# Kernel tuning notes

Hardware: AMD Instinct MI355X
Metric: run time of the kernel (lower is better)

## Reference

```python
import jax, jax.numpy as jnp
import numpy as np


def _lstm(x, Wx, Wh, b):
    """Fused-gate LSTM over time axis 1. x: [B,T,I]; Wx: [I,4H]; Wh: [H,4H]; b: [4H].
    Gate order (i, f, g, o) as in flax.linen.LSTMCell. Zero initial carry."""
    B, T, _ = x.shape
    H = Wh.shape[0]
    # Precompute all input-to-gate contributions in one big GEMM.
    xg = jnp.einsum('bti,ih->bth', x, Wx) + b  # [B,T,4H]

    def step(carry, xt):
        c, h = carry
        z = xt + h @ Wh  # [B,4H]
        i, f, g, o = jnp.split(z, 4, axis=-1)
        c = jax.nn.sigmoid(f) * c + jax.nn.sigmoid(i) * jnp.tanh(g)
        h = jax.nn.sigmoid(o) * jnp.tanh(c)
        return (c, h), h

    init = (jnp.zeros((B, H), x.dtype), jnp.zeros((B, H), x.dtype))
    _, hs = jax.lax.scan(step, init, jnp.swapaxes(xg, 0, 1))  # hs: [T,B,H]
    return jnp.swapaxes(hs, 0, 1)  # [B,T,H]


def _forward(X, conv_w, conv_b,
             Wx1, Wh1, b1, Wx2, Wh2, b2, Wx3, Wh3, b3, Wx4, Wh4, b4,
             Wa, ba, Va, bva, Wd1, bd1, Wd2, bd2):
    # 1-D conv, SAME padding (flax default), NWC layout.
    x = jax.lax.conv_general_dilated(X, conv_w, (1,), 'SAME',
                                     dimension_numbers=('NWC', 'WIO', 'NWC')) + conv_b
    # NOTE: source uses jnp.flip(..., axis=-1) -> flips FEATURE axis (faithful to source).
    x1 = _lstm(x, Wx1, Wh1, b1)
    x2 = _lstm(jnp.flip(x, axis=-1), Wx2, Wh2, b2)
    x = jnp.concatenate([x1, x2], axis=-1)  # [B,T,2F]
    x1 = _lstm(x, Wx3, Wh3, b3)
    x2 = _lstm(jnp.flip(x, axis=-1), Wx4, Wh4, b4)
    enc = jnp.concatenate([x1, x2], axis=-1)  # [B,T,4F]
    # Additive attention: softmax over time axis.
    score = jnp.tanh(enc @ Wa + ba) @ Va + bva  # [B,T,1]
    w = jax.nn.softmax(score, axis=1)
    ctx = jnp.sum(w * enc, axis=1)  # [B,4F]
    # MLP head (dropout deterministic -> identity).
    h = jnp.tanh(ctx @ Wd1 + bd1)
    return h @ Wd2 + bd2  # [B,1]


def setup_inputs() -> dict:
    key = jax.random.key(0)
    B, T, Cin, F = 32, 4096, 8, 64
    ks = iter(jax.random.split(key, 32))

    def w(shape):
        fan_in = shape[0] if len(shape) <= 2 else shape[0] * shape[1]
        return jax.random.normal(next(ks), shape, jnp.float32) / np.sqrt(fan_in)

    d = {}
    d['X'] = jax.random.normal(next(ks), (B, T, Cin), jnp.float32)
    d['conv_w'] = w((4, Cin, 16))
    d['conv_b'] = jnp.zeros((16,), jnp.float32)
    lstm_dims = {'1': (16, F), '2': (16, F), '3': (2 * F, 2 * F), '4': (2 * F, 2 * F)}
    for n, (i_dim, h_dim) in lstm_dims.items():
        d['Wx' + n] = w((i_dim, 4 * h_dim))
        d['Wh' + n] = w((h_dim, 4 * h_dim))
        d['b' + n] = jnp.zeros((4 * h_dim,), jnp.float32)
    d['Wa'] = w((4 * F, F)); d['ba'] = jnp.zeros((F,), jnp.float32)
    d['Va'] = w((F, 1));     d['bva'] = jnp.zeros((1,), jnp.float32)
    d['Wd1'] = w((4 * F, F)); d['bd1'] = jnp.zeros((F,), jnp.float32)
    d['Wd2'] = w((F, 1));     d['bd2'] = jnp.zeros((1,), jnp.float32)
    d['deterministic'] = 1
    return d


def reference(X, conv_w, conv_b,
              Wx1, Wh1, b1, Wx2, Wh2, b2, Wx3, Wh3, b3, Wx4, Wh4, b4,
              Wa, ba, Va, bva, Wd1, bd1, Wd2, bd2, deterministic):
    # deterministic=1 -> dropout is the identity; already reflected in _forward.
    return _forward(X, conv_w, conv_b,
                    Wx1, Wh1, b1, Wx2, Wh2, b2, Wx3, Wh3, b3, Wx4, Wh4, b4,
                    Wa, ba, Va, bva, Wd1, bd1, Wd2, bd2)
```

## Files before the change

kernel.cpp:

```cpp
#include <hip/hip_runtime.h>


#define TFULL 4096
#define NB 32

__device__ __forceinline__ float fexp2(float x){ return __builtin_amdgcn_exp2f(x); }
__device__ __forceinline__ float frcp(float x){ return __builtin_amdgcn_rcpf(x); }
__device__ __forceinline__ float sigf(float x){ return frcp(1.f + fexp2(-1.44269504f*x)); }
__device__ __forceinline__ float tanh_(float x){
    float e = fexp2(fminf(2.88539008f*x, 126.f));
    return (e - 1.f) * frcp(e + 1.f);
}
#define PIN4(v) asm volatile("" : "+v"(v.x), "+v"(v.y), "+v"(v.z), "+v"(v.w))

__global__ __launch_bounds__(256) void k_init(float* __restrict__ st1,
        float* __restrict__ st2, float* __restrict__ am, float* __restrict__ al,
        float* __restrict__ acc){
    int i = blockIdx.x * 256 + threadIdx.x;
    if (i < 8192)  st1[i] = 0.f;
    if (i < 16384) st2[i] = 0.f;
    if (i < 8192)  acc[i] = 0.f;
    if (i < 32){ am[i] = -3.4e38f; al[i] = 0.f; }
}

__global__ __launch_bounds__(256) void k_pack(
        const float* __restrict__ Wx1, const float* __restrict__ Wh1, const float* __restrict__ b1,
        const float* __restrict__ Wx2, const float* __restrict__ Wh2, const float* __restrict__ b2,
        const float* __restrict__ Wx3, const float* __restrict__ Wh3, const float* __restrict__ b3,
        const float* __restrict__ Wx4, const float* __restrict__ Wh4, const float* __restrict__ b4,
        float* __restrict__ W34, float* __restrict__ b34, float* __restrict__ W2p,
        float* __restrict__ W1p, float* __restrict__ b12i){
    int i0 = blockIdx.x * 256 + threadIdx.x;
    int stride = gridDim.x * 256;
    for (int e = i0; e < 131072; e += stride){
        int k = e >> 10, n = e & 1023;
        int l = n >> 9, nn = n & 511, j = nn >> 2, g = nn & 3;
        W34[e] = l ? Wx4[(127 - k)*512 + g*128 + j] : Wx3[k*512 + g*128 + j];
    }
    for (int e = i0; e < 1024; e += stride){
        int l = e >> 9, nn = e & 511, j = nn >> 2, g = nn & 3;
        b34[e] = (l ? b4 : b3)[g*128 + j];
    }
    for (int e = i0; e < 131072; e += stride){
        int l = e >> 16, r = e & 65535, tid = r >> 6, widx = r & 63;
        int q = tid & 127, s = tid >> 7;
        int m = widx >> 4, kk = widx & 15;
        W2p[e] = (l ? Wh4 : Wh3)[(16*s + kk)*512 + m*128 + q];
    }
    for (int e = i0; e < 49152; e += stride){
        int l = e / 24576, r = e % 24576, tid = r / 48, widx = r % 48;
        int q = tid & 63, s = tid >> 6;
        int m = widx / 12, rem = widx % 12, k4 = rem >> 2, cmp = rem & 3;
        float v = 0.f;
        if (k4 < 2){
            v = (l ? Wh2 : Wh1)[(8*s + k4*4 + cmp)*256 + m*64 + q];
        } else if (s < 4){
            int rr = 4*s + cmp;
            v = l ? Wx2[(15 - rr)*256 + m*64 + q] : Wx1[rr*256 + m*64 + q];
        }
        W1p[e] = v;
    }
    for (int e = i0; e < 512; e += stride){
        int l = e >> 8, nn = e & 255, j = nn >> 2, g = nn & 3;
        b12i[e] = (l ? b2 : b1)[g*64 + j];
    }
}

__global__ __launch_bounds__(256) void k_conv(const float* __restrict__ X,
        const float* __restrict__ W, const float* __restrict__ Bv,
        float* __restrict__ out, int t0, int lc){
    __shared__ float Ws[512];
    __shared__ float bs[16];
    int tid = threadIdx.x;
    Ws[tid] = W[tid]; Ws[tid + 256] = W[tid + 256];
    if (tid < 16) bs[tid] = Bv[tid];
    __syncthreads();
    int m = blockIdx.x * 256 + tid;
    int b = m >> lc, trel = m & ((1 << lc) - 1);
    int t = t0 + trel;
    float o[16];
    #pragma unroll
    for (int co = 0; co < 16; ++co) o[co] = bs[co];
    #pragma unroll
    for (int w = 0; w < 4; ++w){
        int tt = t + w - 1;
        if (tt >= 0 && tt < TFULL){
            const float* xr = X + ((size_t)(b << 12) + tt) * 8;
            #pragma unroll
            for (int ci = 0; ci < 8; ++ci){
                float v = xr[ci];
                #pragma unroll
                for (int co = 0; co < 16; ++co) o[co] += v * Ws[(w*8 + ci)*16 + co];
            }
        }
    }
    float* op = out + (size_t)m * 16;
    #pragma unroll
    for (int q = 0; q < 4; ++q)
        *(float4*)(op + q*4) = make_float4(o[q*4], o[q*4+1], o[q*4+2], o[q*4+3]);
}

__global__ void __launch_bounds__(512)
k_scan1(const float* __restrict__ x, const float* __restrict__ W1p,
        const float* __restrict__ b12i,
        float* __restrict__ cc, float* __restrict__ st1, int C){
    int l = blockIdx.x >> 5;
    int b = blockIdx.x & 31;
    int tid = threadIdx.x;
    int q = tid & 63;
    int s = tid >> 6;
    float4 w[12];
    {
        const float4* wp = (const float4*)(W1p + ((size_t)l*512 + tid)*48);
        #pragma unroll
        for (int i = 0; i < 12; ++i) w[i] = wp[i];
        #pragma unroll
        for (int i = 0; i < 12; ++i) PIN4(w[i]);
    }
    float4 bi4 = make_float4(0.f, 0.f, 0.f, 0.f);
    if (tid < 64) bi4 = *(const float4*)(b12i + l*256 + tid*4);

    __shared__ float xs[128 * 16];
    __shared__ float zp1[8 * 256];
    __shared__ float ccbuf[128 * 64];
    __shared__ float hbufs[64];
    float c = 0.f;
    int sidx = (l*32 + b)*64 + q;
    if (tid < 64){ c = st1[sidx]; hbufs[tid] = st1[4096 + sidx]; }
    __syncthreads();

    const float* xb = x + ((size_t)b * C) * 16;
    float* ccb = cc + ((size_t)b * C) * 128 + (l << 6);
    int BS = C < 128 ? C : 128;
    int bsm = BS - 1;
    int fr = tid >> 2, fi = tid & 3;

    #pragma clang loop unroll(disable)
    for (int t = 0; t < C; ++t){
        int st = t & bsm;
        if (st == 0){
            __syncthreads();
            if (t && fr < BS){
                const float4* cb4 = (const float4*)ccbuf + fr*16 + fi*4;
                float4* cgp = (float4*)(ccb + (size_t)(t - BS + fr)*128) + fi*4;
                #pragma unroll
                for (int i = 0; i < 4; ++i) cgp[i] = cb4[i];
            }
            if (tid < BS*4)
                ((float4*)xs)[tid] = ((const float4*)(xb + (size_t)t*16))[tid];
            __syncthreads();
        }
        float a0 = 0.f, a1 = 0.f, a2 = 0.f, a3 = 0.f;
        const float4* hb4 = (const float4*)hbufs + (s << 1);
        #pragma unroll
        for (int k4 = 0; k4 < 2; ++k4){
            float4 hv = hb4[k4];
            a0 = fmaf(hv.x, w[k4].x, a0);     a0 = fmaf(hv.y, w[k4].y, a0);
            a0 = fmaf(hv.z, w[k4].z, a0);     a0 = fmaf(hv.w, w[k4].w, a0);
            a1 = fmaf(hv.x, w[3+k4].x, a1);   a1 = fmaf(hv.y, w[3+k4].y, a1);
            a1 = fmaf(hv.z, w[3+k4].z, a1);   a1 = fmaf(hv.w, w[3+k4].w, a1);
            a2 = fmaf(hv.x, w[6+k4].x, a2);   a2 = fmaf(hv.y, w[6+k4].y, a2);
            a2 = fmaf(hv.z, w[6+k4].z, a2);   a2 = fmaf(hv.w, w[6+k4].w, a2);
            a3 = fmaf(hv.x, w[9+k4].x, a3);   a3 = fmaf(hv.y, w[9+k4].y, a3);
            a3 = fmaf(hv.z, w[9+k4].z, a3);   a3 = fmaf(hv.w, w[9+k4].w, a3);
        }
        if (s < 4){
            float4 xv = ((const float4*)(xs + st * 16))[s];
            a0 = fmaf(xv.x, w[2].x, a0);    a0 = fmaf(xv.y, w[2].y, a0);
            a0 = fmaf(xv.z, w[2].z, a0);    a0 = fmaf(xv.w, w[2].w, a0);
            a1 = fmaf(xv.x, w[5].x, a1);    a1 = fmaf(xv.y, w[5].y, a1);
            a1 = fmaf(xv.z, w[5].z, a1);    a1 = fmaf(xv.w, w[5].w, a1);
            a2 = fmaf(xv.x, w[8].x, a2);    a2 = fmaf(xv.y, w[8].y, a2);
            a2 = fmaf(xv.z, w[8].z, a2);    a2 = fmaf(xv.w, w[8].w, a2);
            a3 = fmaf(xv.x, w[11].x, a3);   a3 = fmaf(xv.y, w[11].y, a3);
            a3 = fmaf(xv.z, w[11].z, a3);   a3 = fmaf(xv.w, w[11].w, a3);
        }
        *(float4*)(zp1 + (s << 8) + (q << 2)) = make_float4(a0, a1, a2, a3);
        __syncthreads();
        if (tid < 64){
            float4 z = bi4;
            #pragma unroll
            for (int ss = 0; ss < 8; ++ss){
                float4 p = *(const float4*)(zp1 + (ss << 8) + (q << 2));
                z.x += p.x; z.y += p.y; z.z += p.z; z.w += p.w;
            }
            float gi = sigf(z.x), gf = sigf(z.y), gg = tanh_(z.z), go = sigf(z.w);
            c = gf * c + gi * gg;
            float h = go * tanh_(c);
            hbufs[tid] = h;
            ccbuf[st*64 + tid] = h;
        }
        __syncthreads();
    }
    if (fr < BS){
        const float4* cb4 = (const float4*)ccbuf + fr*16 + fi*4;
        float4* cgp = (float4*)(ccb + (size_t)(C - BS + fr)*128) + fi*4;
        #pragma unroll
        for (int i = 0; i < 4; ++i) cgp[i] = cb4[i];
    }
    if (tid < 64){ st1[sidx] = c; st1[4096 + sidx] = hbufs[tid]; }
}

template<bool TANH>
__global__ __launch_bounds__(128) void k_gemm(
        const float* __restrict__ A, int lda,
        const float* __restrict__ B, int ldb,
        const float* __restrict__ bias,
        float* __restrict__ Cm, int ldc, int K){
    __shared__ float As[64 * 129];
    __shared__ float Bs[64 * 68];
    int tid = threadIdx.x;
    int tx = tid & 7;
    int ty = tid >> 3;
    int r0 = blockIdx.x * 128;
    int n0 = blockIdx.y * 64;
    float acc[8][8];
    #pragma unroll
    for (int i = 0; i < 8; ++i)
        #pragma unroll
        for (int n = 0; n < 8; ++n) acc[i][n] = 0.f;

    for (int kb = 0; kb < K; kb += 64){
        __syncthreads();
        for (int idx = tid; idx < 2048; idx += 128){
            int r = idx >> 4, k4 = idx & 15;
            float4 v = *(const float4*)(A + (size_t)(r0 + r) * lda + kb + k4*4);
            As[(k4*4 + 0)*129 + r] = v.x;
            As[(k4*4 + 1)*129 + r] = v.y;
            As[(k4*4 + 2)*129 + r] = v.z;
            As[(k4*4 + 3)*129 + r] = v.w;
        }
        for (int idx = tid; idx < 1024; idx += 128){
            int n4 = idx & 15, k = idx >> 4;
            float4 v = *(const float4*)(B + (size_t)(kb + k) * ldb + n0 + n4*4);
            *(float4*)(Bs + k*68 + n4*4) = v;
        }
        __syncthreads();
        #pragma unroll 4
        for (int k = 0; k < 64; ++k){
            float a[8];
            #pragma unroll
            for (int i = 0; i < 8; ++i) a[i] = As[k*129 + ty*8 + i];
            float4 b0 = *(const float4*)(Bs + k*68 + tx*8);
            float4 b1 = *(const float4*)(Bs + k*68 + tx*8 + 4);
            float bq[8] = {b0.x, b0.y, b0.z, b0.w, b1.x, b1.y, b1.z, b1.w};
            #pragma unroll
            for (int i = 0; i < 8; ++i)
                #pragma unroll
                for (int n = 0; n < 8; ++n) acc[i][n] += a[i] * bq[n];
        }
    }
    #pragma unroll
    for (int i = 0; i < 8; ++i){
        size_t rr = (size_t)r0 + ty*8 + i;
        float* cp = Cm + rr * ldc + n0 + tx*8;
        float ov[8];
        #pragma unroll
        for (int n = 0; n < 8; ++n){
            float v = acc[i][n] + bias[n0 + tx*8 + n];
            ov[n] = TANH ? tanh_(v) : v;
        }
        *(float4*)cp       = make_float4(ov[0], ov[1], ov[2], ov[3]);
        *(float4*)(cp + 4) = make_float4(ov[4], ov[5], ov[6], ov[7]);
    }
}

__global__ void __launch_bounds__(1024)
k_scan2(const float* __restrict__ xg, const float* __restrict__ W2p,
        float* __restrict__ enc, float* __restrict__ st2, int C){
    int l = blockIdx.x >> 5;
    int b = blockIdx.x & 31;
    int tid = threadIdx.x;
    int q = tid & 127;
    int s = tid >> 7;
    float4 w[16];
    {
        const float4* wp = (const float4*)(W2p + ((size_t)l*1024 + tid)*64);
        #pragma unroll
        for (int i = 0; i < 16; ++i) w[i] = wp[i];
        #pragma unroll
        for (int i = 0; i < 16; ++i) PIN4(w[i]);
    }

    __shared__ float xgbuf[32 * 512];
    __shared__ float zp[8 * 512];
    __shared__ float encbuf[32 * 128];
    __shared__ float hbufs[128];

    float c = 0.f;
    int sidx = (l*32 + b)*128 + q;
    if (tid < 128){ c = st2[sidx]; hbufs[tid] = st2[8192 + sidx]; }
    __syncthreads();

    const float* xgg = xg + ((size_t)b * C) * 1024 + (l << 9);
    float* encb = enc + ((size_t)b * C) * 256 + (l << 7);
    int tq = tid & 31, tr = tid >> 5;

    #pragma clang loop unroll(disable)
    for (int t = 0; t < C; ++t){
        int st = t & 31;
        if (st == 0){
            __syncthreads();
            if (t){
                float4 ev = *(const float4*)(encbuf + tr*128 + tq*4);
                *(float4*)(encb + (size_t)(t - 32 + tr) * 256 + tq*4) = ev;
            }
            {
                const float4* src = (const float4*)(xgg + (size_t)(t + tr) * 1024);
                float4* xb4 = (float4*)(xgbuf + tr*512);
                #pragma unroll
                for (int i = 0; i < 4; ++i) xb4[tq + 32*i] = src[tq + 32*i];
            }
            __syncthreads();
        }
        float a0 = 0.f, a1 = 0.f, a2 = 0.f, a3 = 0.f;
        const float4* hb4 = (const float4*)hbufs + (s << 2);
        #pragma unroll
        for (int k4 = 0; k4 < 4; ++k4){
            float4 hv = hb4[k4];
            a0 = fmaf(hv.x, w[k4].x, a0);      a0 = fmaf(hv.y, w[k4].y, a0);
            a0 = fmaf(hv.z, w[k4].z, a0);      a0 = fmaf(hv.w, w[k4].w, a0);
            a1 = fmaf(hv.x, w[4+k4].x, a1);    a1 = fmaf(hv.y, w[4+k4].y, a1);
            a1 = fmaf(hv.z, w[4+k4].z, a1);    a1 = fmaf(hv.w, w[4+k4].w, a1);
            a2 = fmaf(hv.x, w[8+k4].x, a2);    a2 = fmaf(hv.y, w[8+k4].y, a2);
            a2 = fmaf(hv.z, w[8+k4].z, a2);    a2 = fmaf(hv.w, w[8+k4].w, a2);
            a3 = fmaf(hv.x, w[12+k4].x, a3);   a3 = fmaf(hv.y, w[12+k4].y, a3);
            a3 = fmaf(hv.z, w[12+k4].z, a3);   a3 = fmaf(hv.w, w[12+k4].w, a3);
        }
        *(float4*)(zp + (s << 9) + (q << 2)) = make_float4(a0, a1, a2, a3);
        __syncthreads();
        if (tid < 128){
            float4 z = *(const float4*)(xgbuf + (st << 9) + (q << 2));
            #pragma unroll
            for (int ss = 0; ss < 8; ++ss){
                float4 p = *(const float4*)(zp + (ss << 9) + (q << 2));
                z.x += p.x; z.y += p.y; z.z += p.z; z.w += p.w;
            }
            float gi = sigf(z.x), gf = sigf(z.y), gg = tanh_(z.z), go = sigf(z.w);
            c = gf * c + gi * gg;
            float h = go * tanh_(c);
            hbufs[tid] = h;
            encbuf[st*128 + tid] = h;
        }
        __syncthreads();
    }
    {
        float4 ev = *(const float4*)(encbuf + tr*128 + tq*4);
        *(float4*)(encb + (size_t)(C - 32 + tr) * 256 + tq*4) = ev;
    }
    if (tid < 128){ st2[sidx] = c; st2[8192 + sidx] = hbufs[tid]; }
}

__global__ __launch_bounds__(256) void k_scorev(const float* __restrict__ u,
        const float* __restrict__ Va, const float* __restrict__ bva,
        float* __restrict__ sc){
    int m = blockIdx.x * 256 + threadIdx.x;
    const float4* up = (const float4*)(u + (size_t)m * 64);
    const float4* vp = (const float4*)Va;
    float acc = 0.f;
    #pragma unroll
    for (int i = 0; i < 16; ++i){
        float4 v = up[i], w = vp[i];
        acc += v.x*w.x + v.y*w.y + v.z*w.z + v.w*w.w;
    }
    sc[m] = acc + bva[0];
}

__global__ __launch_bounds__(1024) void k_attn(const float* __restrict__ sc,
        const float* __restrict__ enc, float* __restrict__ am,
        float* __restrict__ al, float* __restrict__ acc, int C){
    int b = blockIdx.x, tid = threadIdx.x;
    __shared__ float es[1024];
    __shared__ float red[16];
    __shared__ float sh[2];
    const float* sp = sc + (size_t)b * C;
    float mloc = -3.4e38f;
    for (int t = tid; t < C; t += 1024) mloc = fmaxf(mloc, sp[t]);
    #pragma unroll
    for (int off = 32; off; off >>= 1) mloc = fmaxf(mloc, __shfl_down(mloc, off));
    if ((tid & 63) == 0) red[tid >> 6] = mloc;
    __syncthreads();
    if (tid == 0){
        float mc = -3.4e38f;
        #pragma unroll
        for (int i = 0; i < 16; ++i) mc = fmaxf(mc, red[i]);
        float mo = am[b];
        float mn = fmaxf(mo, mc);
        sh[0] = mn;
        sh[1] = fexp2(1.44269504f * (mo - mn));
        am[b] = mn;
    }
    __syncthreads();
    float mn = sh[0], alpha = sh[1];
    float eloc = 0.f;
    for (int t = tid; t < C; t += 1024){
        float e = fexp2(1.44269504f * (sp[t] - mn));
        es[t] = e; eloc += e;
    }
    #pragma unroll
    for (int off = 32; off; off >>= 1) eloc += __shfl_down(eloc, off);
    if ((tid & 63) == 0) red[tid >> 6] = eloc;
    __syncthreads();
    if (tid == 0){
        float sm = 0.f;
        #pragma unroll
        for (int i = 0; i < 16; ++i) sm += red[i];
        al[b] = al[b] * alpha + sm;
    }
    int jf = tid & 255, sl = tid >> 8;
    int tlen = C >> 2;
    const float* ep = enc + ((size_t)b * C + (size_t)sl * tlen) * 256 + jf;
    const float* eb = es + sl * tlen;
    float a = 0.f;
    for (int t = 0; t < tlen; ++t) a = fmaf(eb[t], ep[(size_t)t * 256], a);
    __syncthreads();
    es[tid] = a;
    __syncthreads();
    if (tid < 256)
        acc[b*256 + tid] = acc[b*256 + tid] * alpha
                         + ((es[tid] + es[256 + tid]) + (es[512 + tid] + es[768 + tid]));
}

__global__ __launch_bounds__(256) void k_head(const float* __restrict__ acc,
        const float* __restrict__ al,
        const float* __restrict__ Wd1, const float* __restrict__ bd1,
        const float* __restrict__ Wd2, const float* __restrict__ bd2,
        float* __restrict__ out){
    __shared__ float ctxs[32 * 256];
    __shared__ float h1s[32 * 64];
    int tid = threadIdx.x;
    for (int idx = tid; idx < 8192; idx += 256){
        int b = idx >> 8;
        ctxs[idx] = acc[idx] / al[b];
    }
    __syncthreads();
    for (int idx = tid; idx < 2048; idx += 256){
        int b = idx >> 6, n = idx & 63;
        float a = bd1[n];
        for (int i = 0; i < 256; ++i) a += ctxs[b*256 + i] * Wd1[i*64 + n];
        h1s[idx] = tanh_(a);
    }
    __syncthreads();
    if (tid < 32){
        float a = bd2[0];
        #pragma unroll
        for (int n = 0; n < 64; ++n) a += h1s[tid*64 + n] * Wd2[n];
        out[tid] = a;
    }
}

extern "C" void kernel_launch(void* const* d_in, const int* in_sizes, int n_in,
                              void* d_out, int out_size, void* d_ws, size_t ws_size,
                              hipStream_t stream){
    const float* X     = (const float*)d_in[0];
    const float* convw = (const float*)d_in[1];
    const float* convb = (const float*)d_in[2];
    const float* Wx1 = (const float*)d_in[3];
    const float* Wh1 = (const float*)d_in[4];
    const float* b1  = (const float*)d_in[5];
    const float* Wx2 = (const float*)d_in[6];
    const float* Wh2 = (const float*)d_in[7];
    const float* b2  = (const float*)d_in[8];
    const float* Wx3 = (const float*)d_in[9];
    const float* Wh3 = (const float*)d_in[10];
    const float* b3  = (const float*)d_in[11];
    const float* Wx4 = (const float*)d_in[12];
    const float* Wh4 = (const float*)d_in[13];
    const float* b4  = (const float*)d_in[14];
    const float* Wa  = (const float*)d_in[15];
    const float* ba  = (const float*)d_in[16];
    const float* Va  = (const float*)d_in[17];
    const float* bva = (const float*)d_in[18];
    const float* Wd1 = (const float*)d_in[19];
    const float* bd1 = (const float*)d_in[20];
    const float* Wd2 = (const float*)d_in[21];
    const float* bd2 = (const float*)d_in[22];
    float* out = (float*)d_out;
    (void)in_sizes; (void)n_in; (void)out_size;

    const size_t fixedFl = 131072 + 1024 + 131072 + 49152 + 512
                         + 8192 + 16384 + 32 + 32 + 8192 + 32*1024;
    size_t capFl = ws_size / 4;
    int C = 1024;
    while (C > 32){
        size_t need = fixedFl + (size_t)NB * C * (16 + 128 + 1024 + 256 + 64);
        if (need <= capFl) break;
        C >>= 1;
    }
    int lc = 31 - __builtin_clz((unsigned)C);
    int nch = TFULL / C;

    float* ws   = (float*)d_ws;
    float* W34  = ws;
    float* b34  = W34 + 131072;
    float* W2p  = b34 + 1024;
    float* W1p  = W2p + 131072;
    float* b12i = W1p + 49152;
    float* st1  = b12i + 512;
    float* st2  = st1 + 8192;
    float* am   = st2 + 16384;
    float* al   = am + 32;
    float* acc  = al + 32;
    float* scb  = acc + 8192;
    float* xcv  = scb + 32*1024;
    float* ccb  = xcv + (size_t)NB*C*16;
    float* xgb  = ccb + (size_t)NB*C*128;
    float* enb  = xgb + (size_t)NB*C*1024;
    float* ub   = enb + (size_t)NB*C*256;

    k_init<<<64, 256, 0, stream>>>(st1, st2, am, al, acc);
    k_pack<<<512, 256, 0, stream>>>(Wx1, Wh1, b1, Wx2, Wh2, b2,
                                    Wx3, Wh3, b3, Wx4, Wh4, b4,
                                    W34, b34, W2p, W1p, b12i);

    for (int ch = 0; ch < nch; ++ch){
        int t0 = ch * C;
        k_conv<<<NB*C/256, 256, 0, stream>>>(X, convw, convb, xcv, t0, lc);
        k_scan1<<<64, 512, 0, stream>>>(xcv, W1p, b12i, ccb, st1, C);
        k_gemm<false><<<dim3(NB*C/128, 16), 128, 0, stream>>>(
            ccb, 128, W34, 1024, b34, xgb, 1024, 128);
        k_scan2<<<64, 1024, 0, stream>>>(xgb, W2p, enb, st2, C);
        k_gemm<true><<<dim3(NB*C/128, 1), 128, 0, stream>>>(
            enb, 256, Wa, 64, ba, ub, 64, 256);
        k_scorev<<<NB*C/256, 256, 0, stream>>>(ub, Va, bva, scb);
        k_attn<<<32, 1024, 0, stream>>>(scb, enb, am, al, acc, C);
    }
    k_head<<<1, 256, 0, stream>>>(acc, al, Wd1, bd1, Wd2, bd2, out);
}
```

Measured before the change: 6.011 ms.

## Replace LDS partial-sum reduction in LSTM scans with wave shuffles and double-buffered h

Both recurrent scan kernels now split the hidden-state dot product across 4 lanes within a wavefront and reduce with xor shuffles instead of writing partials to shared memory and summing them in a second phase. The hidden state is double-buffered so each timestep needs a single barrier instead of two, and the block size is halved while each thread keeps twice as many weights in registers. This targets per-step barrier and LDS round-trip latency on the serial critical path. In exchange it raises register pressure and leaves three of every four lanes idle during the gate nonlinearities.

```diff
diff --git a/kernel.cpp b/kernel.cpp
--- a/kernel.cpp
+++ b/kernel.cpp
@@ -42,21 +42,25 @@
         b34[e] = (l ? b4 : b3)[g*128 + j];
     }
     for (int e = i0; e < 131072; e += stride){
-        int l = e >> 16, r = e & 65535, tid = r >> 6, widx = r & 63;
-        int q = tid & 127, s = tid >> 7;
-        int m = widx >> 4, kk = widx & 15;
-        W2p[e] = (l ? Wh4 : Wh3)[(16*s + kk)*512 + m*128 + q];
-    }
-    for (int e = i0; e < 49152; e += stride){
-        int l = e / 24576, r = e % 24576, tid = r / 48, widx = r % 48;
-        int q = tid & 63, s = tid >> 6;
-        int m = widx / 12, rem = widx % 12, k4 = rem >> 2, cmp = rem & 3;
-        float v = 0.f;
-        if (k4 < 2){
-            v = (l ? Wh2 : Wh1)[(8*s + k4*4 + cmp)*256 + m*64 + q];
-        } else if (s < 4){
-            int rr = 4*s + cmp;
-            v = l ? Wx2[(15 - rr)*256 + m*64 + q] : Wx1[rr*256 + m*64 + q];
+        int l = e >> 16, r = e & 65535, tid = r >> 7, widx = r & 127;
+        int g = widx >> 5, kk = widx & 31;
+        int wv = tid >> 6, lam = tid & 63;
+        int c = lam & 15, s4 = lam >> 4;
+        int J = 16*wv + c;
+        W2p[e] = (l ? Wh4 : Wh3)[(32*s4 + kk)*512 + g*128 + J];
+    }
+    for (int e = i0; e < 40960; e += stride){
+        int l = e / 20480, r = e % 20480, tid = r / 80, widx = r % 80;
+        int g = widx / 20, rem = widx % 20, kk4 = rem >> 2, cmp = rem & 3;
+        int wv = tid >> 6, lam = tid & 63;
+        int c = lam & 15, s4 = lam >> 4;
+        int J = 16*wv + c;
+        float v;
+        if (kk4 < 4){
+            v = (l ? Wh2 : Wh1)[(16*s4 + 4*kk4 + cmp)*256 + g*64 + J];
+        } else {
+            int rr = 4*s4 + cmp;
+            v = l ? Wx2[(15 - rr)*256 + g*64 + J] : Wx1[rr*256 + g*64 + J];
         }
         W1p[e] = v;
     }
@@ -100,105 +104,116 @@
         *(float4*)(op + q*4) = make_float4(o[q*4], o[q*4+1], o[q*4+2], o[q*4+3]);
 }
 
-__global__ void __launch_bounds__(512)
+__global__ void __launch_bounds__(256)
 k_scan1(const float* __restrict__ x, const float* __restrict__ W1p,
         const float* __restrict__ b12i,
         float* __restrict__ cc, float* __restrict__ st1, int C){
     int l = blockIdx.x >> 5;
     int b = blockIdx.x & 31;
     int tid = threadIdx.x;
-    int q = tid & 63;
-    int s = tid >> 6;
-    float4 w[12];
+    int lam = tid & 63, wv = tid >> 6;
+    int cq = lam & 15, s4 = lam >> 4;
+    int J = 16*wv + cq;
+    float4 w[20];
     {
-        const float4* wp = (const float4*)(W1p + ((size_t)l*512 + tid)*48);
-        #pragma unroll
-        for (int i = 0; i < 12; ++i) w[i] = wp[i];
-        #pragma unroll
-        for (int i = 0; i < 12; ++i) PIN4(w[i]);
+        const float4* wp = (const float4*)(W1p + ((size_t)l*256 + tid)*80);
+        #pragma unroll
+        for (int i = 0; i < 20; ++i) w[i] = wp[i];
+        #pragma unroll
+        for (int i = 0; i < 20; ++i) PIN4(w[i]);
     }
     float4 bi4 = make_float4(0.f, 0.f, 0.f, 0.f);
-    if (tid < 64) bi4 = *(const float4*)(b12i + l*256 + tid*4);
+    if (s4 == 0) bi4 = *(const float4*)(b12i + l*256 + 4*J);
 
     __shared__ float xs[128 * 16];
-    __shared__ float zp1[8 * 256];
     __shared__ float ccbuf[128 * 64];
-    __shared__ float hbufs[64];
-    float c = 0.f;
-    int sidx = (l*32 + b)*64 + q;
-    if (tid < 64){ c = st1[sidx]; hbufs[tid] = st1[4096 + sidx]; }
+    __shared__ float hb[2][64];
+    float cst = 0.f;
+    int base = (l*32 + b)*64;
+    if (s4 == 0) cst = st1[base + J];
+    if (tid < 64) hb[0][tid] = st1[4096 + base + tid];
     __syncthreads();
 
     const float* xb = x + ((size_t)b * C) * 16;
     float* ccb = cc + ((size_t)b * C) * 128 + (l << 6);
     int BS = C < 128 ? C : 128;
     int bsm = BS - 1;
-    int fr = tid >> 2, fi = tid & 3;
 
     #pragma clang loop unroll(disable)
     for (int t = 0; t < C; ++t){
         int st = t & bsm;
         if (st == 0){
             __syncthreads();
-            if (t && fr < BS){
-                const float4* cb4 = (const float4*)ccbuf + fr*16 + fi*4;
-                float4* cgp = (float4*)(ccb + (size_t)(t - BS + fr)*128) + fi*4;
+            if (t){
                 #pragma unroll
-                for (int i = 0; i < 4; ++i) cgp[i] = cb4[i];
+                for (int i = 0; i < 8; ++i){
+                    int Qi = tid + i*256;
+                    if (Qi < BS*16){
+                        int row = Qi >> 4, qr = Qi & 15;
+                        *((float4*)(ccb + (size_t)(t - BS + row)*128) + qr) =
+                            ((const float4*)ccbuf)[Qi];
+                    }
+                }
             }
-            if (tid < BS*4)
-                ((float4*)xs)[tid] = ((const float4*)(xb + (size_t)t*16))[tid];
+            #pragma unroll
+            for (int i = 0; i < 2; ++i){
+                int Qi = tid + i*256;
+                if (Qi < BS*4)
+                    ((float4*)xs)[Qi] = ((const float4*)(xb + (size_t)t*16))[Qi];
+            }
             __syncthreads();
         }
-        float a0 = 0.f, a1 = 0.f, a2 = 0.f, a3 = 0.f;
-        const float4* hb4 = (const float4*)hbufs + (s << 1);
-        #pragma unroll
-        for (int k4 = 0; k4 < 2; ++k4){
-            float4 hv = hb4[k4];
+        const float* hcur = hb[t & 1];
+        float a0, a1, a2, a3;
+        {
+            float4 xv = *(const float4*)(xs + st*16 + 4*s4);
+            a0 = xv.x*w[4].x;  a0 = fmaf(xv.y, w[4].y, a0);
+            a0 = fmaf(xv.z, w[4].z, a0);   a0 = fmaf(xv.w, w[4].w, a0);
+            a1 = xv.x*w[9].x;  a1 = fmaf(xv.y, w[9].y, a1);
+            a1 = fmaf(xv.z, w[9].z, a1);   a1 = fmaf(xv.w, w[9].w, a1);
+            a2 = xv.x*w[14].x; a2 = fmaf(xv.y, w[14].y, a2);
+            a2 = fmaf(xv.z, w[14].z, a2);  a2 = fmaf(xv.w, w[14].w, a2);
+            a3 = xv.x*w[19].x; a3 = fmaf(xv.y, w[19].y, a3);
+            a3 = fmaf(xv.z, w[19].z, a3);  a3 = fmaf(xv.w, w[19].w, a3);
+        }
+        #pragma unroll
+        for (int k4 = 0; k4 < 4; ++k4){
+            float4 hv = *(const float4*)(hcur + 16*s4 + 4*k4);
             a0 = fmaf(hv.x, w[k4].x, a0);     a0 = fmaf(hv.y, w[k4].y, a0);
             a0 = fmaf(hv.z, w[k4].z, a0);     a0 = fmaf(hv.w, w[k4].w, a0);
-            a1 = fmaf(hv.x, w[3+k4].x, a1);   a1 = fmaf(hv.y, w[3+k4].y, a1);
-            a1 = fmaf(hv.z, w[3+k4].z, a1);   a1 = fmaf(hv.w, w[3+k4].w, a1);
-            a2 = fmaf(hv.x, w[6+k4].x, a2);   a2 = fmaf(hv.y, w[6+k4].y, a2);
-            a2 = fmaf(hv.z, w[6+k4].z, a2);   a2 = fmaf(hv.w, w[6+k4].w, a2);
-            a3 = fmaf(hv.x, w[9+k4].x, a3);   a3 = fmaf(hv.y, w[9+k4].y, a3);
-            a3 = fmaf(hv.z, w[9+k4].z, a3);   a3 = fmaf(hv.w, w[9+k4].w, a3);
-        }
-        if (s < 4){
-            float4 xv = ((const float4*)(xs + st * 16))[s];
-            a0 = fmaf(xv.x, w[2].x, a0);    a0 = fmaf(xv.y, w[2].y, a0);
-            a0 = fmaf(xv.z, w[2].z, a0);    a0 = fmaf(xv.w, w[2].w, a0);
-            a1 = fmaf(xv.x, w[5].x, a1);    a1 = fmaf(xv.y, w[5].y, a1);
-            a1 = fmaf(xv.z, w[5].z, a1);    a1 = fmaf(xv.w, w[5].w, a1);
-            a2 = fmaf(xv.x, w[8].x, a2);    a2 = fmaf(xv.y, w[8].y, a2);
-            a2 = fmaf(xv.z, w[8].z, a2);    a2 = fmaf(xv.w, w[8].w, a2);
-            a3 = fmaf(xv.x, w[11].x, a3);   a3 = fmaf(xv.y, w[11].y, a3);
-            a3 = fmaf(xv.z, w[11].z, a3);   a3 = fmaf(xv.w, w[11].w, a3);
-        }
-        *(float4*)(zp1 + (s << 8) + (q << 2)) = make_float4(a0, a1, a2, a3);
+            a1 = fmaf(hv.x, w[5+k4].x, a1);   a1 = fmaf(hv.y, w[5+k4].y, a1);
+            a1 = fmaf(hv.z, w[5+k4].z, a1);   a1 = fmaf(hv.w, w[5+k4].w, a1);
+            a2 = fmaf(hv.x, w[10+k4].x, a2);  a2 = fmaf(hv.y, w[10+k4].y, a2);
+            a2 = fmaf(hv.z, w[10+k4].z, a2);  a2 = fmaf(hv.w, w[10+k4].w, a2);
+            a3 = fmaf(hv.x, w[15+k4].x, a3);  a3 = fmaf(hv.y, w[15+k4].y, a3);
+            a3 = fmaf(hv.z, w[15+k4].z, a3);  a3 = fmaf(hv.w, w[15+k4].w, a3);
+        }
+        a0 += __shfl_xor(a0, 16); a0 += __shfl_xor(a0, 32);
+        a1 += __shfl_xor(a1, 16); a1 += __shfl_xor(a1, 32);
+        a2 += __shfl_xor(a2, 16); a2 += __shfl_xor(a2, 32);
+        a3 += __shfl_xor(a3, 16); a3 += __shfl_xor(a3, 32);
+        if (s4 == 0){
+            float zi = a0 + bi4.x, zf = a1 + bi4.y, zg = a2 + bi4.z, zo = a3 + bi4.w;
+            cst = sigf(zf) * cst + sigf(zi) * tanh_(zg);
+            float h = sigf(zo) * tanh_(cst);
+            hb[(t + 1) & 1][J] = h;
+            ccbuf[st*64 + J] = h;
+        }
         __syncthreads();
-        if (tid < 64){
-            float4 z = bi4;
-            #pragma unroll
-            for (int ss = 0; ss < 8; ++ss){
-                float4 p = *(const float4*)(zp1 + (ss << 8) + (q << 2));
-                z.x += p.x; z.y += p.y; z.z += p.z; z.w += p.w;
+    }
+    {
+        #pragma unroll
+        for (int i = 0; i < 8; ++i){
+            int Qi = tid + i*256;
+            if (Qi < BS*16){
+                int row = Qi >> 4, qr = Qi & 15;
+                *((float4*)(ccb + (size_t)(C - BS + row)*128) + qr) =
+                    ((const float4*)ccbuf)[Qi];
             }
-            float gi = sigf(z.x), gf = sigf(z.y), gg = tanh_(z.z), go = sigf(z.w);
-            c = gf * c + gi * gg;
-            float h = go * tanh_(c);
-            hbufs[tid] = h;
-            ccbuf[st*64 + tid] = h;
-        }
-        __syncthreads();
-    }
-    if (fr < BS){
-        const float4* cb4 = (const float4*)ccbuf + fr*16 + fi*4;
-        float4* cgp = (float4*)(ccb + (size_t)(C - BS + fr)*128) + fi*4;
-        #pragma unroll
-        for (int i = 0; i < 4; ++i) cgp[i] = cb4[i];
-    }
-    if (tid < 64){ st1[sidx] = c; st1[4096 + sidx] = hbufs[tid]; }
+        }
+    }
+    if (s4 == 0) st1[base + J] = cst;
+    if (tid < 64) st1[4096 + base + tid] = hb[C & 1][tid];
 }
 
 template<bool TANH>
@@ -265,36 +280,37 @@
     }
 }
 
-__global__ void __launch_bounds__(1024)
+__global__ void __launch_bounds__(512)
 k_scan2(const float* __restrict__ xg, const float* __restrict__ W2p,
         float* __restrict__ enc, float* __restrict__ st2, int C){
     int l = blockIdx.x >> 5;
     int b = blockIdx.x & 31;
     int tid = threadIdx.x;
-    int q = tid & 127;
-    int s = tid >> 7;
-    float4 w[16];
+    int lam = tid & 63, wv = tid >> 6;
+    int cq = lam & 15, s4 = lam >> 4;
+    int J = 16*wv + cq;
+    float4 w[32];
     {
-        const float4* wp = (const float4*)(W2p + ((size_t)l*1024 + tid)*64);
-        #pragma unroll
-        for (int i = 0; i < 16; ++i) w[i] = wp[i];
-        #pragma unroll
-        for (int i = 0; i < 16; ++i) PIN4(w[i]);
+        const float4* wp = (const float4*)(W2p + ((size_t)l*512 + tid)*128);
+        #pragma unroll
+        for (int i = 0; i < 32; ++i) w[i] = wp[i];
+        #pragma unroll
+        for (int i = 0; i < 32; ++i) PIN4(w[i]);
     }
 
     __shared__ float xgbuf[32 * 512];
-    __shared__ float zp[8 * 512];
     __shared__ float encbuf[32 * 128];
-    __shared__ float hbufs[128];
-
-    float c = 0.f;
-    int sidx = (l*32 + b)*128 + q;
-    if (tid < 128){ c = st2[sidx]; hbufs[tid] = st2[8192 + sidx]; }
+    __shared__ float hb[2][160];
+    float cst = 0.f;
+    int base = (l*32 + b)*128;
+    if (s4 == 0) cst = st2[base + J];
+    if (tid < 128) hb[0][tid + 4*(tid >> 5)] = st2[8192 + base + tid];
     __syncthreads();
 
     const float* xgg = xg + ((size_t)b * C) * 1024 + (l << 9);
     float* encb = enc + ((size_t)b * C) * 256 + (l << 7);
-    int tq = tid & 31, tr = tid >> 5;
+    int hoff = 36*s4;
+    int joff = J + 4*(J >> 5);
 
     #pragma clang loop unroll(disable)
     for (int t = 0; t < C; ++t){
@@ -302,53 +318,62 @@
         if (st == 0){
             __syncthreads();
             if (t){
-                float4 ev = *(const float4*)(encbuf + tr*128 + tq*4);
-                *(float4*)(encb + (size_t)(t - 32 + tr) * 256 + tq*4) = ev;
+                #pragma unroll
+                for (int i = 0; i < 2; ++i){
+                    int Qi = tid + i*512;
+                    int row = Qi >> 5, qr = Qi & 31;
+                    *((float4*)(encb + (size_t)(t - 32 + row)*256) + qr) =
+                        ((const float4*)encbuf)[Qi];
+                }
             }
-            {
-                const float4* src = (const float4*)(xgg + (size_t)(t + tr) * 1024);
-                float4* xb4 = (float4*)(xgbuf + tr*512);
-                #pragma unroll
-                for (int i = 0; i < 4; ++i) xb4[tq + 32*i] = src[tq + 32*i];
+            #pragma unroll
+            for (int i = 0; i < 8; ++i){
+                int Qi = tid + i*512;
+                int row = Qi >> 7, qr = Qi & 127;
+                ((float4*)xgbuf)[Qi] =
+                    *((const float4*)(xgg + (size_t)(t + row)*1024) + qr);
             }
             __syncthreads();
         }
+        const float* hcur = hb[t & 1];
         float a0 = 0.f, a1 = 0.f, a2 = 0.f, a3 = 0.f;
-        const float4* hb4 = (const float4*)hbufs + (s << 2);
-        #pragma unroll
-        for (int k4 = 0; k4 < 4; ++k4){
-            float4 hv = hb4[k4];
+        #pragma unroll
+        for (int k4 = 0; k4 < 8; ++k4){
+            float4 hv = *(const float4*)(hcur + hoff + 4*k4);
             a0 = fmaf(hv.x, w[k4].x, a0);      a0 = fmaf(hv.y, w[k4].y, a0);
             a0 = fmaf(hv.z, w[k4].z, a0);      a0 = fmaf(hv.w, w[k4].w, a0);
-            a1 = fmaf(hv.x, w[4+k4].x, a1);    a1 = fmaf(hv.y, w[4+k4].y, a1);
-            a1 = fmaf(hv.z, w[4+k4].z, a1);    a1 = fmaf(hv.w, w[4+k4].w, a1);
-            a2 = fmaf(hv.x, w[8+k4].x, a2);    a2 = fmaf(hv.y, w[8+k4].y, a2);
-            a2 = fmaf(hv.z, w[8+k4].z, a2);    a2 = fmaf(hv.w, w[8+k4].w, a2);
-            a3 = fmaf(hv.x, w[12+k4].x, a3);   a3 = fmaf(hv.y, w[12+k4].y, a3);
-            a3 = fmaf(hv.z, w[12+k4].z, a3);   a3 = fmaf(hv.w, w[12+k4].w, a3);
-        }
-        *(float4*)(zp + (s << 9) + (q << 2)) = make_float4(a0, a1, a2, a3);
+            a1 = fmaf(hv.x, w[8+k4].x, a1);    a1 = fmaf(hv.y, w[8+k4].y, a1);
+            a1 = fmaf(hv.z, w[8+k4].z, a1);    a1 = fmaf(hv.w, w[8+k4].w, a1);
+            a2 = fmaf(hv.x, w[16+k4].x, a2);   a2 = fmaf(hv.y, w[16+k4].y, a2);
+            a2 = fmaf(hv.z, w[16+k4].z, a2);   a2 = fmaf(hv.w, w[16+k4].w, a2);
+            a3 = fmaf(hv.x, w[24+k4].x, a3);   a3 = fmaf(hv.y, w[24+k4].y, a3);
+            a3 = fmaf(hv.z, w[24+k4].z, a3);   a3 = fmaf(hv.w, w[24+k4].w, a3);
+        }
+        a0 += __shfl_xor(a0, 16); a0 += __shfl_xor(a0, 32);
+        a1 += __shfl_xor(a1, 16); a1 += __shfl_xor(a1, 32);
+        a2 += __shfl_xor(a2, 16); a2 += __shfl_xor(a2, 32);
+        a3 += __shfl_xor(a3, 16); a3 += __shfl_xor(a3, 32);
+        if (s4 == 0){
+            float4 xq = *(const float4*)(xgbuf + st*512 + 4*J);
+            float zi = a0 + xq.x, zf = a1 + xq.y, zg = a2 + xq.z, zo = a3 + xq.w;
+            cst = sigf(zf) * cst + sigf(zi) * tanh_(zg);
+            float h = sigf(zo) * tanh_(cst);
+            hb[(t + 1) & 1][joff] = h;
+            encbuf[st*128 + J] = h;
+        }
         __syncthreads();
-        if (tid < 128){
-            float4 z = *(const float4*)(xgbuf + (st << 9) + (q << 2));
-            #pragma unroll
-            for (int ss = 0; ss < 8; ++ss){
-                float4 p = *(const float4*)(zp + (ss << 9) + (q << 2));
-                z.x += p.x; z.y += p.y; z.z += p.z; z.w += p.w;
-            }
-            float gi = sigf(z.x), gf = sigf(z.y), gg = tanh_(z.z), go = sigf(z.w);
-            c = gf * c + gi * gg;
-            float h = go * tanh_(c);
-            hbufs[tid] = h;
-            encbuf[st*128 + tid] = h;
-        }
-        __syncthreads();
     }
     {
-        float4 ev = *(const float4*)(encbuf + tr*128 + tq*4);
-        *(float4*)(encb + (size_t)(C - 32 + tr) * 256 + tq*4) = ev;
-    }
-    if (tid < 128){ st2[sidx] = c; st2[8192 + sidx] = hbufs[tid]; }
+        #pragma unroll
+        for (int i = 0; i < 2; ++i){
+            int Qi = tid + i*512;
+            int row = Qi >> 5, qr = Qi & 31;
+            *((float4*)(encb + (size_t)(C - 32 + row)*256) + qr) =
+                ((const float4*)encbuf)[Qi];
+        }
+    }
+    if (s4 == 0) st2[base + J] = cst;
+    if (tid < 128) st2[8192 + base + tid] = hb[C & 1][tid + 4*(tid >> 5)];
 }
 
 __global__ __launch_bounds__(256) void k_scorev(const float* __restrict__ u,
@@ -478,7 +503,7 @@
     float* out = (float*)d_out;
     (void)in_sizes; (void)n_in; (void)out_size;
 
-    const size_t fixedFl = 131072 + 1024 + 131072 + 49152 + 512
+    const size_t fixedFl = 131072 + 1024 + 131072 + 40960 + 512
                          + 8192 + 16384 + 32 + 32 + 8192 + 32*1024;
     size_t capFl = ws_size / 4;
     int C = 1024;
@@ -495,7 +520,7 @@
     float* b34  = W34 + 131072;
     float* W2p  = b34 + 1024;
     float* W1p  = W2p + 131072;
-    float* b12i = W1p + 49152;
+    float* b12i = W1p + 40960;
     float* st1  = b12i + 512;
     float* st2  = st1 + 8192;
     float* am   = st2 + 16384;
@@ -516,10 +541,10 @@
     for (int ch = 0; ch < nch; ++ch){
         int t0 = ch * C;
         k_conv<<<NB*C/256, 256, 0, stream>>>(X, convw, convb, xcv, t0, lc);
-        k_scan1<<<64, 512, 0, stream>>>(xcv, W1p, b12i, ccb, st1, C);
+        k_scan1<<<64, 256, 0, stream>>>(xcv, W1p, b12i, ccb, st1, C);
         k_gemm<false><<<dim3(NB*C/128, 16), 128, 0, stream>>>(
             ccb, 128, W34, 1024, b34, xgb, 1024, 128);
-        k_scan2<<<64, 1024, 0, stream>>>(xgb, W2p, enb, st2, C);
+        k_scan2<<<64, 512, 0, stream>>>(xgb, W2p, enb, st2, C);
         k_gemm<true><<<dim3(NB*C/128, 1), 128, 0, stream>>>(
             enb, 256, Wa, 64, ba, ub, 64, 256);
         k_scorev<<<NB*C/256, 256, 0, stream>>>(ub, Va, bva, scb);
```

New measurement: 6.024 ms. About the same (+0.2%).
